# Performance work log

Measured on AMD Instinct MI355X. Metric: run time of the kernel, lower is better.

The kernel has to match this reference:

```python
import jax, jax.numpy as jnp
import numpy as np

N, E, F_IN, H = 100000, 3200000, 256, 32

def gcn_conv(x, src, dst, w, W, b):
    # PyG GCNConv with edge weights and added self-loops (weight 1), symmetric norm
    xw = x @ W                                                # [N, H]
    deg = jax.ops.segment_sum(w, dst, num_segments=N) + 1.0   # includes self-loop
    dis = jax.lax.rsqrt(deg)                                  # deg >= 1, safe
    norm = dis[src] * w * dis[dst]                            # [E]
    agg = jax.ops.segment_sum(norm[:, None] * xw[src], dst, num_segments=N)
    agg = agg + (dis * dis)[:, None] * xw                     # self-loop term
    return agg + b


def setup_inputs() -> dict:
    key = jax.random.key(0)
    ks = jax.random.split(key, 20)
    z = lambda n: jnp.zeros((n,), jnp.float32)
    p = lambda i, shape, s: jax.random.normal(ks[i], shape, jnp.float32) * s
    return {
        "x": jax.random.normal(ks[0], (N, F_IN), jnp.float32),
        "edge_index": jax.random.randint(ks[1], (2, E), 0, N),
        "edge_weight": jax.random.uniform(ks[2], (E,), jnp.float32),
        "prev_hidden_state": jax.random.normal(ks[3], (N, H), jnp.float32),
        # GCNConv weights (stored [in, out]) + post-aggregation biases
        "W_z": p(4, (F_IN, H), 0.05), "b_z": z(H),
        "W_r": p(5, (F_IN, H), 0.05), "b_r": z(H),
        "W_h": p(6, (F_IN, H), 0.05), "b_h": z(H),
        # GRU gate linears Linear(2H, H), stored [2H, H]
        "Lz_W": p(7, (2 * H, H), 0.1), "Lz_b": z(H),
        "Lr_W": p(8, (2 * H, H), 0.1), "Lr_b": z(H),
        "Lh_W": p(9, (2 * H, H), 0.1), "Lh_b": z(H),
        # readout Linear(H, 1)
        "head_W": p(10, (H, 1), 0.1), "head_b": z(1),
    }


def reference(x, edge_index, edge_weight, prev_hidden_state,
              W_z, b_z, W_r, b_r, W_h, b_h,
              Lz_W, Lz_b, Lr_W, Lr_b, Lh_W, Lh_b,
              head_W, head_b):
    src, dst = edge_index[0], edge_index[1]
    Hp = prev_hidden_state
    Z = jax.nn.sigmoid(
        jnp.concatenate([gcn_conv(x, src, dst, edge_weight, W_z, b_z), Hp], 1) @ Lz_W + Lz_b)
    R = jax.nn.sigmoid(
        jnp.concatenate([gcn_conv(x, src, dst, edge_weight, W_r, b_r), Hp], 1) @ Lr_W + Lr_b)
    H_tilde = jnp.tanh(
        jnp.concatenate([gcn_conv(x, src, dst, edge_weight, W_h, b_h), Hp * R], 1) @ Lh_W + Lh_b)
    h = Z * Hp + (1.0 - Z) * H_tilde
    y = jax.nn.relu(h) @ head_W + head_b
    return (y, h)
```

## Files before the change

kernel.cpp:

```cpp
#include <hip/hip_runtime.h>
#include <math.h>

#define N_NODES 100000
#define F_INDIM 256
#define NB 391
#define BCAP 9216

__device__ __forceinline__ unsigned bf16pack(float a, float b) {
  unsigned ua = __float_as_uint(a);
  ua += 0x7FFFu + ((ua >> 16) & 1u);
  unsigned ub = __float_as_uint(b);
  ub += 0x7FFFu + ((ub >> 16) & 1u);
  return (ub & 0xFFFF0000u) | (ua >> 16);
}
__device__ __forceinline__ float lo16(unsigned v) { return __uint_as_float(v << 16); }
__device__ __forceinline__ float hi16(unsigned v) { return __uint_as_float(v & 0xFFFF0000u); }

using bf16x8 = __attribute__((ext_vector_type(8))) short;
using f32x4  = __attribute__((ext_vector_type(4))) float;

__global__ __launch_bounds__(512) void gemm_bin(
    const float* __restrict__ x,
    const float* __restrict__ Wz, const float* __restrict__ Wr, const float* __restrict__ Wh,
    unsigned* __restrict__ XWb,
    const int* __restrict__ ei, const float* __restrict__ w,
    int* __restrict__ bucketCursor, uint2* __restrict__ staged, int E) {
  __shared__ unsigned smem[12672];
  const int t = threadIdx.x;
  const int m = blockIdx.x % 5;
  if (m < 2) {
    int* lc    = (int*)smem;
    int* lbase = (int*)smem + 512;
    if (t < NB) lc[t] = 0;
    __syncthreads();
    const int bid = (blockIdx.x / 5) * 2 + m;
    const int base = bid * 6144;
#pragma unroll
    for (int i = 0; i < 12; i++) {
      int e = base + i * 512 + t;
      if (e < E) atomicAdd(&lc[((unsigned)ei[E + e]) >> 8], 1);
    }
    __syncthreads();
    if (t < NB) {
      int c = lc[t];
      lbase[t] = c ? atomicAdd(&bucketCursor[t], c) : 0;
    }
    __syncthreads();
    if (t < NB) lc[t] = 0;
    __syncthreads();
#pragma unroll
    for (int i = 0; i < 12; i++) {
      int e = base + i * 512 + t;
      if (e < E) {
        unsigned dst = (unsigned)ei[E + e];
        int b = dst >> 8;
        int r = lbase[b] + atomicAdd(&lc[b], 1);
        if (r < BCAP)
          staged[(size_t)b * BCAP + r] =
              make_uint2((unsigned)ei[e] | ((dst & 255u) << 17), __float_as_uint(w[e]));
      }
    }
    return;
  }
  const int gid = (blockIdx.x / 5) * 3 + (m - 2);
  const int row0 = gid * 128;
  if (row0 >= N_NODES) return;
  ushort* sWt = (ushort*)smem;
  {
    const float* Ws[3] = {Wz, Wr, Wh};
#pragma unroll
    for (int mm = 0; mm < 3; mm++) {
      const float* Wp = Ws[mm];
      for (int i = t; i < 8192; i += 512) {
        int k = i >> 5, c = i & 31;
        unsigned uv = __float_as_uint(Wp[i]);
        uv += 0x7FFFu + ((uv >> 16) & 1u);
        sWt[(mm * 32 + c) * 264 + k] = (ushort)(uv >> 16);
      }
    }
  }
  __syncthreads();
  const int wv = t >> 6;
  const int l = t & 63;
  const int nl = l & 15;
  const int kg = l >> 4;
  int arow = row0 + wv * 16 + nl;
  int arowc = arow < N_NODES ? arow : N_NODES - 1;
  f32x4 acc[6];
#pragma unroll
  for (int c = 0; c < 6; c++) acc[c] = (f32x4){0.f, 0.f, 0.f, 0.f};
  const float* xrow = x + (size_t)arowc * F_INDIM + kg * 8;
#pragma unroll
  for (int ks = 0; ks < 8; ks++) {
    float4 xa = *(const float4*)(xrow + ks * 32);
    float4 xb = *(const float4*)(xrow + ks * 32 + 4);
    uint4 au;
    au.x = bf16pack(xa.x, xa.y);
    au.y = bf16pack(xa.z, xa.w);
    au.z = bf16pack(xb.x, xb.y);
    au.w = bf16pack(xb.z, xb.w);
    bf16x8 af = *(bf16x8*)&au;
#pragma unroll
    for (int c = 0; c < 6; c++) {
      const ushort* bp = sWt + (c * 16 + nl) * 264 + ks * 32 + kg * 8;
      bf16x8 bf = *(const bf16x8*)bp;
      acc[c] = __builtin_amdgcn_mfma_f32_16x16x32_bf16(af, bf, acc[c], 0, 0, 0);
    }
  }
#pragma unroll
  for (int c = 0; c < 6; c++) {
#pragma unroll
    for (int r = 0; r < 4; r++) {
      float v = acc[c][r];
      float o = __shfl_xor(v, 1);
      int orow = row0 + wv * 16 + kg * 4 + r;
      if ((nl & 1) == 0 && orow < N_NODES)
        XWb[(size_t)orow * 48 + c * 8 + (nl >> 1)] = bf16pack(v, o);
    }
  }
}

__global__ __launch_bounds__(256) void finalize(
    const uint2* __restrict__ staged, const int* __restrict__ bucketCursor,
    uint2* __restrict__ e2, int* __restrict__ rowstart, int* __restrict__ cntA,
    float* __restrict__ dis) {
  __shared__ int fc[256];
  __shared__ float fd[256];
  __shared__ int fscan[256];
  __shared__ int fcur[256];
  const int t = threadIdx.x;
  const int b = blockIdx.x;
  const size_t lo = (size_t)b * BCAP;
  int M = bucketCursor[b]; if (M > BCAP) M = BCAP;
  fc[t] = 0; fd[t] = 0.f;
  __syncthreads();
  for (int i = t; i < M; i += 256) {
    uint2 ed = staged[lo + i];
    int fl = (ed.x >> 17) & 255;
    atomicAdd(&fc[fl], 1);
    atomicAdd(&fd[fl], __uint_as_float(ed.y));
  }
  __syncthreads();
  int v = fc[t];
  fscan[t] = v;
  __syncthreads();
  for (int off = 1; off < 256; off <<= 1) {
    int xv = (t >= off) ? fscan[t - off] : 0;
    __syncthreads();
    fscan[t] += xv;
    __syncthreads();
  }
  int excl = fscan[t] - v;
  int node = (b << 8) + t;
  if (node < N_NODES) {
    rowstart[node] = (int)lo + excl;
    cntA[node] = v;
    dis[node] = rsqrtf(fd[t] + 1.0f);
  }
  fcur[t] = excl;
  __syncthreads();
  for (int i = t; i < M; i += 256) {
    uint2 ed = staged[lo + i];
    int fl = (ed.x >> 17) & 255;
    int p = atomicAdd(&fcur[fl], 1);
    e2[lo + p] = make_uint2(ed.x & 0x1FFFFu, ed.y);
  }
}

#define FMA8(vv, nn)                                              \
  a0 = fmaf(nn, lo16(vv.x), a0); a1 = fmaf(nn, hi16(vv.x), a1);   \
  a2 = fmaf(nn, lo16(vv.y), a2); a3 = fmaf(nn, hi16(vv.y), a3);   \
  a4 = fmaf(nn, lo16(vv.z), a4); a5 = fmaf(nn, hi16(vv.z), a5);   \
  a6 = fmaf(nn, lo16(vv.w), a6); a7 = fmaf(nn, hi16(vv.w), a7);

__global__ __launch_bounds__(256, 6) void gru_gather(
    const uint2* __restrict__ e2, const int* __restrict__ rowstart,
    const int* __restrict__ cnt, const unsigned* __restrict__ XWb,
    const float* __restrict__ dis, const float* __restrict__ Hp,
    const float* __restrict__ bz, const float* __restrict__ br, const float* __restrict__ bh,
    const float* __restrict__ LzW, const float* __restrict__ Lzb,
    const float* __restrict__ LrW, const float* __restrict__ Lrb,
    const float* __restrict__ LhW, const float* __restrict__ Lhb,
    const float* __restrict__ hW, const float* __restrict__ hb,
    float* __restrict__ outY, float* __restrict__ outH, int N) {
  __shared__ unsigned sLz[1024], sLr[1024], sLh[1024];
  __shared__ float aggTmp[4][5][96];
  __shared__ float sb96[96];
  __shared__ float sLzb[32], sLrb[32], sLhb[32], shW[32];
  __shared__ float2 sg2[4][48];
  __shared__ float shp[4][32], shr[4][32];
  __shared__ float shb;
  const int t = threadIdx.x;
  for (int i = t; i < 1024; i += 256) {
    int jj = i & 31, k2 = i >> 5;
    sLz[i] = bf16pack(LzW[(2 * k2) * 32 + jj], LzW[(2 * k2 + 1) * 32 + jj]);
    sLr[i] = bf16pack(LrW[(2 * k2) * 32 + jj], LrW[(2 * k2 + 1) * 32 + jj]);
    sLh[i] = bf16pack(LhW[(2 * k2) * 32 + jj], LhW[(2 * k2 + 1) * 32 + jj]);
  }
  if (t < 32) {
    sb96[t] = bz[t]; sb96[32 + t] = br[t]; sb96[64 + t] = bh[t];
    sLzb[t] = Lzb[t]; sLrb[t] = Lrb[t]; sLhb[t] = Lhb[t]; shW[t] = hW[t];
  }
  if (t == 0) shb = hb[0];
  __syncthreads();
  const int ws = t >> 6;
  const int l = t & 63;
  const int lp = (l < 48) ? l : 47;
  const int j = l & 31;
  const int half = l >> 5;
  const int sl = (l < 60) ? (l / 12) : 4;
  const int q  = (l < 60) ? (l % 12) : 11;
  const float* sgf = (const float*)&sg2[ws][0];
  int wid = blockIdx.x * 4 + ws;
  int nw = gridDim.x * 4;
  for (int n = wid; n < N; n += nw) {
    const int start = rowstart[n];
    const int c = cnt[n];
    const float d = dis[n];
    float a0 = 0.f, a1 = 0.f, a2 = 0.f, a3 = 0.f;
    float a4 = 0.f, a5 = 0.f, a6 = 0.f, a7 = 0.f;
    for (int e0 = 0; e0 < c; e0 += 60) {
      int srcv = 0; float pw = 0.f;
      if (l < 60 && e0 + l < c) {
        uint2 ed = e2[start + e0 + l];
        srcv = (int)ed.x;
        pw = __uint_as_float(ed.y) * dis[srcv];
      }
      int mm = c - e0; if (mm > 60) mm = 60;
      for (int k0 = 0; k0 < mm; k0 += 10) {
        int iA = k0 + sl, iB = k0 + 5 + sl;
        int sA = __shfl(srcv, iA), sB = __shfl(srcv, iB);
        float nA = __shfl(pw, iA), nB = __shfl(pw, iB);
        uint4 vA = *(const uint4*)(XWb + sA * 48 + (q << 2));
        uint4 vB = *(const uint4*)(XWb + sB * 48 + (q << 2));
        FMA8(vA, nA);
        FMA8(vB, nB);
      }
    }
    if (l < 60) {
      float4* dst4 = (float4*)&aggTmp[ws][sl][q * 8];
      dst4[0] = make_float4(a0, a1, a2, a3);
      dst4[1] = make_float4(a4, a5, a6, a7);
    }
    float g0 = 0.f, g1 = 0.f;
#pragma unroll
    for (int ss = 0; ss < 5; ss++) {
      float2 v2 = *(const float2*)&aggTmp[ws][ss][2 * lp];
      g0 += v2.x; g1 += v2.y;
    }
    g0 *= d; g1 *= d;
    {
      unsigned v = XWb[n * 48 + lp];
      float d2 = d * d;
      g0 = fmaf(d2, lo16(v), g0) + sb96[2 * lp];
      g1 = fmaf(d2, hi16(v), g1) + sb96[2 * lp + 1];
    }
    if (l < 48) sg2[ws][l] = make_float2(g0, g1);
    float hpj = 0.f;
    if (l < 32) { hpj = Hp[(size_t)n * 32 + l]; shp[ws][l] = hpj; }
    const unsigned* Wm = half ? sLr : sLz;
    const float* gsel = half ? (sgf + 32) : sgf;
    float val = half ? sLrb[j] : sLzb[j];
#pragma unroll
    for (int k2 = 0; k2 < 16; k2++) {
      unsigned wv = Wm[k2 * 32 + j];
      val = fmaf(gsel[2 * k2],     lo16(wv), val);
      val = fmaf(gsel[2 * k2 + 1], hi16(wv), val);
    }
#pragma unroll
    for (int k2 = 16; k2 < 32; k2++) {
      unsigned wv = Wm[k2 * 32 + j];
      val = fmaf(shp[ws][2 * k2 - 32], lo16(wv), val);
      val = fmaf(shp[ws][2 * k2 - 31], hi16(wv), val);
    }
    float gate = 1.f / (1.f + __expf(-val));
    if (half) shr[ws][j] = shp[ws][j] * gate;
    float s = half ? 0.f : sLhb[j];
#pragma unroll
    for (int k2 = 0; k2 < 16; k2++) {
      int kk2 = half ? (k2 + 16) : k2;
      unsigned wv = sLh[kk2 * 32 + j];
      float x0 = half ? shr[ws][2 * k2]     : sgf[64 + 2 * k2];
      float x1 = half ? shr[ws][2 * k2 + 1] : sgf[64 + 2 * k2 + 1];
      s = fmaf(x0, lo16(wv), s);
      s = fmaf(x1, hi16(wv), s);
    }
    s += __shfl_xor(s, 32);
    if (!half) {
      float ht = tanhf(s);
      float h = gate * hpj + (1.f - gate) * ht;
      outH[(size_t)n * 32 + j] = h;
      float cacc = fmaxf(h, 0.f) * shW[j];
#pragma unroll
      for (int off = 16; off > 0; off >>= 1) cacc += __shfl_xor(cacc, off, 32);
      if (j == 0) outY[n] = cacc + shb;
    }
  }
}

extern "C" void kernel_launch(void* const* d_in, const int* in_sizes, int n_in,
                              void* d_out, int out_size, void* d_ws, size_t ws_size,
                              hipStream_t stream) {
  const float* x    = (const float*)d_in[0];
  const int*   ei   = (const int*)d_in[1];
  const float* w    = (const float*)d_in[2];
  const float* Hp   = (const float*)d_in[3];
  const float* Wz   = (const float*)d_in[4];
  const float* bz   = (const float*)d_in[5];
  const float* Wr   = (const float*)d_in[6];
  const float* br   = (const float*)d_in[7];
  const float* Wh   = (const float*)d_in[8];
  const float* bh   = (const float*)d_in[9];
  const float* LzW  = (const float*)d_in[10];
  const float* Lzb  = (const float*)d_in[11];
  const float* LrW  = (const float*)d_in[12];
  const float* Lrb  = (const float*)d_in[13];
  const float* LhW  = (const float*)d_in[14];
  const float* Lhb  = (const float*)d_in[15];
  const float* hW   = (const float*)d_in[16];
  const float* hb   = (const float*)d_in[17];

  const int N = N_NODES;
  const int E = in_sizes[2];

  char* p = (char*)d_ws;
  unsigned* XWb   = (unsigned*)p;  p += (size_t)(N * 48 + 64) * 4;
  uint2*    staged= (uint2*)p;     p += (size_t)NB * BCAP * 8;
  uint2*    e2    = (uint2*)p;     p += (size_t)NB * BCAP * 8;
  int* rowstart   = (int*)p;       p += (size_t)N * 4;
  int* cnt        = (int*)p;       p += (size_t)N * 4;
  float* dis      = (float*)p;     p += (size_t)N * 4;
  int* bucketCursor = (int*)p;     p += (NB + 1) * 4;

  float* outY = (float*)d_out;
  float* outH = outY + N;

  hipMemsetAsync(bucketCursor, 0, (NB + 1) * sizeof(int), stream);

  gemm_bin<<<1305, 512, 0, stream>>>(x, Wz, Wr, Wh, XWb, ei, w,
                                     bucketCursor, staged, E);
  finalize<<<NB, 256, 0, stream>>>(staged, bucketCursor, e2, rowstart, cnt, dis);
  gru_gather<<<1536, 256, 0, stream>>>(e2, rowstart, cnt, XWb, dis, Hp,
                                       bz, br, bh,
                                       LzW, Lzb, LrW, Lrb, LhW, Lhb,
                                       hW, hb, outY, outH, N);
}
```

Before: 232.0 us.

## Use nontemporal loads/stores, cache dst indices, widen finalize blocks

Marks streaming reads (edge indices, weights, x rows, staged edges, Hp) and output writes as nontemporal so they do not pollute cache needed for the XWb gather. The binning pass keeps dst indices in registers instead of reloading them in the second pass, and the finalize kernel moves to 512 threads per block to process each bucket with more parallelism. XWb index math is widened to size_t. These are several loosely related tweaks; nontemporal hints may help or hurt depending on reuse, and the wider finalize block leaves half its threads idle during the scan.

```diff
diff --git a/kernel.cpp b/kernel.cpp
--- a/kernel.cpp
+++ b/kernel.cpp
@@ -18,6 +18,8 @@
 
 using bf16x8 = __attribute__((ext_vector_type(8))) short;
 using f32x4  = __attribute__((ext_vector_type(4))) float;
+using fv4    = __attribute__((ext_vector_type(4))) float;
+typedef unsigned long long ull;
 
 __global__ __launch_bounds__(512) void gemm_bin(
     const float* __restrict__ x,
@@ -35,10 +37,12 @@
     __syncthreads();
     const int bid = (blockIdx.x / 5) * 2 + m;
     const int base = bid * 6144;
+    int dstv[12];
 #pragma unroll
     for (int i = 0; i < 12; i++) {
       int e = base + i * 512 + t;
-      if (e < E) atomicAdd(&lc[((unsigned)ei[E + e]) >> 8], 1);
+      dstv[i] = (e < E) ? __builtin_nontemporal_load(ei + E + e) : -1;
+      if (dstv[i] >= 0) atomicAdd(&lc[((unsigned)dstv[i]) >> 8], 1);
     }
     __syncthreads();
     if (t < NB) {
@@ -51,13 +55,15 @@
 #pragma unroll
     for (int i = 0; i < 12; i++) {
       int e = base + i * 512 + t;
-      if (e < E) {
-        unsigned dst = (unsigned)ei[E + e];
+      if (dstv[i] >= 0) {
+        unsigned dst = (unsigned)dstv[i];
         int b = dst >> 8;
         int r = lbase[b] + atomicAdd(&lc[b], 1);
+        unsigned sv = (unsigned)__builtin_nontemporal_load(ei + e);
+        float wv = __builtin_nontemporal_load(w + e);
         if (r < BCAP)
           staged[(size_t)b * BCAP + r] =
-              make_uint2((unsigned)ei[e] | ((dst & 255u) << 17), __float_as_uint(w[e]));
+              make_uint2(sv | ((dst & 255u) << 17), __float_as_uint(wv));
       }
     }
     return;
@@ -92,13 +98,13 @@
   const float* xrow = x + (size_t)arowc * F_INDIM + kg * 8;
 #pragma unroll
   for (int ks = 0; ks < 8; ks++) {
-    float4 xa = *(const float4*)(xrow + ks * 32);
-    float4 xb = *(const float4*)(xrow + ks * 32 + 4);
+    fv4 xa = __builtin_nontemporal_load((const fv4*)(xrow + ks * 32));
+    fv4 xb = __builtin_nontemporal_load((const fv4*)(xrow + ks * 32 + 4));
     uint4 au;
-    au.x = bf16pack(xa.x, xa.y);
-    au.y = bf16pack(xa.z, xa.w);
-    au.z = bf16pack(xb.x, xb.y);
-    au.w = bf16pack(xb.z, xb.w);
+    au.x = bf16pack(xa[0], xa[1]);
+    au.y = bf16pack(xa[2], xa[3]);
+    au.z = bf16pack(xb[0], xb[1]);
+    au.w = bf16pack(xb[2], xb[3]);
     bf16x8 af = *(bf16x8*)&au;
 #pragma unroll
     for (int c = 0; c < 6; c++) {
@@ -120,7 +126,7 @@
   }
 }
 
-__global__ __launch_bounds__(256) void finalize(
+__global__ __launch_bounds__(512) void finalize(
     const uint2* __restrict__ staged, const int* __restrict__ bucketCursor,
     uint2* __restrict__ e2, int* __restrict__ rowstart, int* __restrict__ cntA,
     float* __restrict__ dis) {
@@ -132,34 +138,36 @@
   const int b = blockIdx.x;
   const size_t lo = (size_t)b * BCAP;
   int M = bucketCursor[b]; if (M > BCAP) M = BCAP;
-  fc[t] = 0; fd[t] = 0.f;
-  __syncthreads();
-  for (int i = t; i < M; i += 256) {
+  if (t < 256) { fc[t] = 0; fd[t] = 0.f; }
+  __syncthreads();
+  for (int i = t; i < M; i += 512) {
     uint2 ed = staged[lo + i];
     int fl = (ed.x >> 17) & 255;
     atomicAdd(&fc[fl], 1);
     atomicAdd(&fd[fl], __uint_as_float(ed.y));
   }
   __syncthreads();
-  int v = fc[t];
-  fscan[t] = v;
+  int v = (t < 256) ? fc[t] : 0;
+  if (t < 256) fscan[t] = v;
   __syncthreads();
   for (int off = 1; off < 256; off <<= 1) {
-    int xv = (t >= off) ? fscan[t - off] : 0;
-    __syncthreads();
-    fscan[t] += xv;
-    __syncthreads();
-  }
-  int excl = fscan[t] - v;
-  int node = (b << 8) + t;
-  if (node < N_NODES) {
-    rowstart[node] = (int)lo + excl;
-    cntA[node] = v;
-    dis[node] = rsqrtf(fd[t] + 1.0f);
-  }
-  fcur[t] = excl;
-  __syncthreads();
-  for (int i = t; i < M; i += 256) {
+    int xv = (t >= off && t < 256) ? fscan[t - off] : 0;
+    __syncthreads();
+    if (t < 256) fscan[t] += xv;
+    __syncthreads();
+  }
+  if (t < 256) {
+    int excl = fscan[t] - v;
+    int node = (b << 8) + t;
+    if (node < N_NODES) {
+      rowstart[node] = (int)lo + excl;
+      cntA[node] = v;
+      dis[node] = rsqrtf(fd[t] + 1.0f);
+    }
+    fcur[t] = excl;
+  }
+  __syncthreads();
+  for (int i = t; i < M; i += 512) {
     uint2 ed = staged[lo + i];
     int fl = (ed.x >> 17) & 255;
     int p = atomicAdd(&fcur[fl], 1);
@@ -222,17 +230,17 @@
     for (int e0 = 0; e0 < c; e0 += 60) {
       int srcv = 0; float pw = 0.f;
       if (l < 60 && e0 + l < c) {
-        uint2 ed = e2[start + e0 + l];
-        srcv = (int)ed.x;
-        pw = __uint_as_float(ed.y) * dis[srcv];
+        ull edv = __builtin_nontemporal_load((const ull*)&e2[start + e0 + l]);
+        srcv = (int)(unsigned)(edv & 0xFFFFFFFFu);
+        pw = __uint_as_float((unsigned)(edv >> 32)) * dis[srcv];
       }
       int mm = c - e0; if (mm > 60) mm = 60;
       for (int k0 = 0; k0 < mm; k0 += 10) {
         int iA = k0 + sl, iB = k0 + 5 + sl;
         int sA = __shfl(srcv, iA), sB = __shfl(srcv, iB);
         float nA = __shfl(pw, iA), nB = __shfl(pw, iB);
-        uint4 vA = *(const uint4*)(XWb + sA * 48 + (q << 2));
-        uint4 vB = *(const uint4*)(XWb + sB * 48 + (q << 2));
+        uint4 vA = *(const uint4*)(XWb + (size_t)sA * 48 + (q << 2));
+        uint4 vB = *(const uint4*)(XWb + (size_t)sB * 48 + (q << 2));
         FMA8(vA, nA);
         FMA8(vB, nB);
       }
@@ -250,14 +258,17 @@
     }
     g0 *= d; g1 *= d;
     {
-      unsigned v = XWb[n * 48 + lp];
+      unsigned v = XWb[(size_t)n * 48 + lp];
       float d2 = d * d;
       g0 = fmaf(d2, lo16(v), g0) + sb96[2 * lp];
       g1 = fmaf(d2, hi16(v), g1) + sb96[2 * lp + 1];
     }
     if (l < 48) sg2[ws][l] = make_float2(g0, g1);
     float hpj = 0.f;
-    if (l < 32) { hpj = Hp[(size_t)n * 32 + l]; shp[ws][l] = hpj; }
+    if (l < 32) {
+      hpj = __builtin_nontemporal_load(&Hp[(size_t)n * 32 + l]);
+      shp[ws][l] = hpj;
+    }
     const unsigned* Wm = half ? sLr : sLz;
     const float* gsel = half ? (sgf + 32) : sgf;
     float val = half ? sLrb[j] : sLzb[j];
@@ -289,11 +300,11 @@
     if (!half) {
       float ht = tanhf(s);
       float h = gate * hpj + (1.f - gate) * ht;
-      outH[(size_t)n * 32 + j] = h;
+      __builtin_nontemporal_store(h, &outH[(size_t)n * 32 + j]);
       float cacc = fmaxf(h, 0.f) * shW[j];
 #pragma unroll
       for (int off = 16; off > 0; off >>= 1) cacc += __shfl_xor(cacc, off, 32);
-      if (j == 0) outY[n] = cacc + shb;
+      if (j == 0) __builtin_nontemporal_store(cacc + shb, &outY[n]);
     }
   }
 }
@@ -339,7 +350,7 @@
 
   gemm_bin<<<1305, 512, 0, stream>>>(x, Wz, Wr, Wh, XWb, ei, w,
                                      bucketCursor, staged, E);
-  finalize<<<NB, 256, 0, stream>>>(staged, bucketCursor, e2, rowstart, cnt, dis);
+  finalize<<<NB, 512, 0, stream>>>(staged, bucketCursor, e2, rowstart, cnt, dis);
   gru_gather<<<1536, 256, 0, stream>>>(e2, rowstart, cnt, XWb, dis, Hp,
                                        bz, br, bh,
                                        LzW, Lzb, LrW, Lrb, LhW, Lhb,
```

After: 253.3 us. 1.09x slower.
